# Optimization experiments

Hardware: AMD Instinct MI355X
Metric: run time of the kernel (lower is better)

## Reference

```python
import jax, jax.numpy as jnp
import numpy as np

CAPACITY = 65536
HIDDEN = 512
NUM_HASHES = 8
HASH_SIZE = 16
BATCH = 2048


def setup_inputs() -> dict:
    key = jax.random.key(0)
    ks = jax.random.split(key, 6)
    scale = 1.0 / np.sqrt(HIDDEN)
    query = jax.random.normal(ks[0], (BATCH, HIDDEN), dtype=jnp.float32)
    memory_keys = jax.random.normal(ks[1], (CAPACITY, HIDDEN), dtype=jnp.float32) * scale
    memory_values = jax.random.normal(ks[2], (CAPACITY, HIDDEN), dtype=jnp.float32) * scale
    hash_projections = jax.random.normal(ks[3], (NUM_HASHES, HIDDEN, HASH_SIZE), dtype=jnp.float32) * scale
    out_w = jax.random.normal(ks[4], (HIDDEN, HIDDEN), dtype=jnp.float32) * scale  # torch Linear weight [out,in]
    out_b = jnp.zeros((HIDDEN,), dtype=jnp.float32)
    return {"query": query, "memory_keys": memory_keys, "memory_values": memory_values,
            "hash_projections": hash_projections, "out_w": out_w, "out_b": out_b, "top_k": 32}


def _compute_hash(x, hash_projections):
    # x: [m, h] -> hash bits [m, num_hashes] in {0,1}
    # einsum 'bh,nhd->bnd' then sum over d then sign-threshold
    proj = jnp.einsum('mh,nhd->mnd', x, hash_projections)
    return (proj.sum(-1) > 0).astype(jnp.int32)


def reference(query, memory_keys, memory_values, hash_projections, out_w, out_b, top_k):
    b, h = query.shape
    q_hash = _compute_hash(query, hash_projections)                    # [b, n]
    k_hash = _compute_hash(memory_keys, hash_projections)              # [c, n] (no_grad in torch)
    # Hamming distance via +/-1 dot product: dot = n - 2*dist (avoids [b,c,n] bool tensor)
    qf = (q_hash * 2 - 1).astype(jnp.float32)
    kf = (k_hash * 2 - 1).astype(jnp.float32)
    dot = jnp.einsum('bn,cn->bc', qf, kf)                              # [b, c]
    hash_dist = ((NUM_HASHES - dot) * 0.5).astype(jnp.int32)           # [b, c]
    k = min(top_k, memory_keys.shape[0])
    _, top_indices = jax.lax.top_k(-hash_dist, k)                      # smallest distances, [b, k]
    selected_keys = memory_keys[top_indices]                           # [b, k, h]
    selected_values = memory_values[top_indices]                       # [b, k, h]
    scores = jnp.einsum('bh,bkh->bk', query, selected_keys) / np.sqrt(h).astype(np.float32)
    attn = jax.nn.softmax(scores, axis=-1)
    memory_output = jnp.einsum('bk,bkh->bh', attn, selected_values)    # [b, h]
    return memory_output @ out_w.T + out_b
```

## Files before the change

### kernel.cpp

```cpp
#include <hip/hip_runtime.h>
#include <stdint.h>

#define BATCH  2048
#define HID    512
#define CAP    65536
#define NHASH  8
#define TOPK   32
#define NSLICE 16
#define SLICE_SZ (CAP / NSLICE)
#define ROWS_TILE 16
#define QTILES (BATCH / ROWS_TILE)
#define KTILES (CAP / ROWS_TILE)
#define QGRID  128
#define KGRID  1024

typedef unsigned int   u32;
typedef unsigned long long u64;
typedef double d4 __attribute__((ext_vector_type(4)));

__global__ __launch_bounds__(256) void k_prep(const float* __restrict__ proj,
                                              double* __restrict__ psumT,
                                              u32* __restrict__ hist16,
                                              const float* __restrict__ w,
                                              float* __restrict__ wt) {
    __shared__ float tile[64][65];
    int bi = blockIdx.x, tid = threadIdx.x;
    if (bi < 2) {
        int g = bi * 256 + tid;
        for (int i = g; i < NSLICE * 256; i += 512) hist16[i] = 0;
        int h = g;
        for (int n = 0; n < NHASH; n++) {
            const float* p = proj + ((size_t)n * HID + h) * 16;
            double s = 0.0;
            #pragma unroll
            for (int d = 0; d < 16; d++) s += (double)p[d];
            psumT[(size_t)h * NHASH + n] = s;
        }
    } else {
        int b = bi - 2, bx = b & 7, by = b >> 3;
        int tx = tid & 63, ty = tid >> 6;
        for (int r = ty; r < 64; r += 4)
            tile[r][tx] = w[(size_t)(by * 64 + r) * HID + bx * 64 + tx];
        __syncthreads();
        for (int r = ty; r < 64; r += 4)
            wt[(size_t)(bx * 64 + r) * HID + by * 64 + tx] = tile[tx][r];
    }
}

__global__ __launch_bounds__(256, 3) void k_hash(const float* __restrict__ query,
                                                 const float* __restrict__ keys,
                                                 const double* __restrict__ psumT,
                                                 unsigned char* __restrict__ qhash,
                                                 unsigned char* __restrict__ khash,
                                                 u32* __restrict__ hist16) {
    __shared__ __align__(16) float sX[ROWS_TILE * HID];
    __shared__ double sAcc4[4][ROWS_TILE][8];

    const int tid  = threadIdx.x;
    const int w    = tid >> 6;
    const int m    = (tid & 63) & 15;
    const int kk   = (tid & 63) >> 4;

    const int isQ = (blockIdx.x < QGRID);
    const float* x        = isQ ? query : keys;
    unsigned char* outb   = isQ ? qhash : khash;
    const int nTiles      = isQ ? QTILES : KTILES;
    const int b0          = isQ ? blockIdx.x : (blockIdx.x - QGRID);
    const int gstride     = isQ ? QGRID : KGRID;
    const int do_hist     = !isQ;

    d4 z = {0.0, 0.0, 0.0, 0.0};
    d4 pr = __builtin_amdgcn_mfma_f64_16x16x4f64((double)(m + 1), 1.0, z, 0, 0, 0);
    d4 pc = __builtin_amdgcn_mfma_f64_16x16x4f64(1.0, (double)(m + 1), z, 0, 0, 0);
    d4 pp = __builtin_amdgcn_mfma_f64_16x16x4f64((double)(1 << kk),
                                                 (double)(1 << (4 * kk)), z, 0, 0, 0);
    int rowOf[4], colOf[4];
    #pragma unroll
    for (int i = 0; i < 4; i++) {
        rowOf[i] = (int)(pr[i] * 0.25) - 1;
        colOf[i] = (int)(pc[i] * 0.25) - 1;
    }
    u32 pb = (u32)pp[0];
    u32 pairPacked = 0;
    #pragma unroll
    for (int e = 0; e < 16; e++)
        if ((pb >> e) & 1u) pairPacked |= (u32)(e & 3) << (2 * (e >> 2));

    const int kAdj = (int)((pairPacked >> (2 * kk)) & 3u);
    double bfrag[32];
    #pragma unroll
    for (int j = 0; j < 32; j++) {
        int kp = 128 * w + 4 * j + kAdj;
        bfrag[j] = (m < 8) ? psumT[(size_t)kp * NHASH + m] : 0.0;
    }

    const int sw = (m & 7) << 2;

    for (int t = b0; t < nTiles; t += gstride) {
        const int rowBase = t * ROWS_TILE;

        for (int i = tid; i < ROWS_TILE * 128; i += 256) {
            int r = i >> 7, G = i & 127;
            float4 v = ((const float4*)(x + (size_t)(rowBase + r) * HID))[G];
            ((float4*)sX)[r * 128 + (G ^ (r & 7))] = v;
        }
        __syncthreads();

        d4 acc = {0.0, 0.0, 0.0, 0.0};
        const float* sxm = sX + m * HID;
        #pragma unroll
        for (int j = 0; j < 32; j++) {
            int k = 128 * w + 4 * j + kk;
            double a = (double)sxm[k ^ sw];
            acc = __builtin_amdgcn_mfma_f64_16x16x4f64(a, bfrag[j], acc, 0, 0, 0);
        }
        #pragma unroll
        for (int i = 0; i < 4; i++) {
            if (((unsigned)rowOf[i] < (unsigned)ROWS_TILE) && ((unsigned)colOf[i] < 8u))
                sAcc4[w][rowOf[i]][colOf[i]] = acc[i];
        }
        __syncthreads();

        if (tid < ROWS_TILE) {
            u32 byte = 0;
            #pragma unroll
            for (int n = 0; n < 8; n++) {
                double s = sAcc4[0][tid][n] + sAcc4[1][tid][n]
                         + sAcc4[2][tid][n] + sAcc4[3][tid][n];
                if (s > 0.0) byte |= (1u << n);
            }
            outb[rowBase + tid] = (unsigned char)byte;
            if (do_hist) atomicAdd(&hist16[((rowBase + tid) / SLICE_SZ) * 256 + byte], 1u);
        }
    }
}

__global__ __launch_bounds__(256) void k_scan(const u32* __restrict__ hist16,
                                              u32* __restrict__ bucketCnt,
                                              u32* __restrict__ bucketOff,
                                              u32* __restrict__ off16) {
    __shared__ u32 wsum[4];
    int v = threadIdx.x, lane = v & 63, wv = v >> 6;
    u32 tot = 0;
    for (int s = 0; s < NSLICE; s++) tot += hist16[s * 256 + v];
    bucketCnt[v] = tot;
    u32 inc = tot;
    #pragma unroll
    for (int s = 1; s < 64; s <<= 1) {
        u32 n = __shfl_up(inc, s, 64);
        if (lane >= s) inc += n;
    }
    if (lane == 63) wsum[wv] = inc;
    __syncthreads();
    u32 wof = 0;
    for (int i = 0; i < wv; i++) wof += wsum[i];
    u32 base = wof + inc - tot;
    bucketOff[v] = base;
    for (int s = 0; s < NSLICE; s++) { off16[s * 256 + v] = base; base += hist16[s * 256 + v]; }
}

__global__ __launch_bounds__(256) void k_compact(const unsigned char* __restrict__ khash,
                                                 const u32* __restrict__ off16,
                                                 u32* __restrict__ bucketList) {
    __shared__ unsigned char sh[SLICE_SZ];
    int s  = blockIdx.x & (NSLICE - 1);
    int bg = blockIdx.x >> 4;
    ((uint4*)sh)[threadIdx.x] = ((const uint4*)(khash + (size_t)s * SLICE_SZ))[threadIdx.x];
    __syncthreads();
    int w = threadIdx.x >> 6, lane = threadIdx.x & 63;
    int v = bg * 4 + w;
    u32 base = off16[s * 256 + v];
    for (int i = 0; i < SLICE_SZ / 64; i++) {
        int c = i * 64 + lane;
        unsigned char byte = sh[c];
        bool hit = (byte == (unsigned char)v);
        u64 m = __ballot(hit);
        if (hit) {
            int rank = __popcll(m & ((1ull << lane) - 1ull));
            bucketList[base + rank] = (u32)(s * SLICE_SZ + c);
        }
        base += (u32)__popcll(m);
    }
}

__global__ __launch_bounds__(256) void k_attn(const float* __restrict__ keys,
                                              const float* __restrict__ vals,
                                              const float* __restrict__ query,
                                              const unsigned char* __restrict__ qhash,
                                              const u32* __restrict__ bucketCnt,
                                              const u32* __restrict__ bucketOff,
                                              const u32* __restrict__ bucketList,
                                              float* __restrict__ mo) {
    __shared__ int sIdx[TOPK];
    __shared__ float sSc[TOPK], sE[TOPK];
    __shared__ int sPos0;
    int b = blockIdx.x, tid = threadIdx.x;
    int w = tid >> 6, lane = tid & 63;

    if (w == 0) {
        if (lane == 0) sPos0 = 0;
        u32 qh = qhash[b];

        int d[4]; u32 cnt[4], off[4];
        #pragma unroll
        for (int jj = 0; jj < 4; jj++) {
            int v = lane + jj * 64;
            d[jj] = __popc(qh ^ (u32)v);
            cnt[jj] = bucketCnt[v];
            off[jj] = bucketOff[v];
        }

        u32 ct[9];
        #pragma unroll
        for (int t = 0; t < 9; t++) {
            u32 c = 0;
            #pragma unroll
            for (int jj = 0; jj < 4; jj++) c += (d[jj] == t) ? cnt[jj] : 0u;
            #pragma unroll
            for (int s = 32; s >= 1; s >>= 1) c += __shfl_xor(c, s, 64);
            ct[t] = c;
        }

        int dcut = 0; u32 run = 0, before = 0;
        for (int t = 0; t < 9; t++) {
            before = run; run += ct[t];
            if (run >= TOPK) { dcut = t; break; }
        }
        int need = TOPK - (int)before;

        #pragma unroll
        for (int jj = 0; jj < 4; jj++) {
            if (d[jj] < dcut && cnt[jj] > 0) {
                int base = atomicAdd(&sPos0, (int)cnt[jj]);
                for (u32 e = 0; e < cnt[jj]; e++)
                    sIdx[base + e] = (int)bucketList[off[jj] + e];
            }
        }

        int nb = 0;
        #pragma unroll
        for (int jj = 0; jj < 4; jj++) nb += (d[jj] == dcut) ? 1 : 0;
        #pragma unroll
        for (int s = 32; s >= 1; s >>= 1) nb += __shfl_xor(nb, s, 64);

        if (nb == 1) {
            u32 boff = 0xFFFFFFFFu;
            #pragma unroll
            for (int jj = 0; jj < 4; jj++) if (d[jj] == dcut) boff = off[jj];
            #pragma unroll
            for (int s = 32; s >= 1; s >>= 1) boff = min(boff, __shfl_xor(boff, s, 64));
            if (lane < need)
                sIdx[(int)before + lane] = (int)bucketList[boff + lane];
        } else {
            u32 pos[4], end[4]; int val[4];
            #pragma unroll
            for (int jj = 0; jj < 4; jj++) {
                if (d[jj] == dcut && cnt[jj] > 0) {
                    pos[jj] = off[jj]; end[jj] = off[jj] + cnt[jj];
                    val[jj] = (int)bucketList[pos[jj]];
                } else { pos[jj] = 0; end[jj] = 0; val[jj] = 0x7fffffff; }
            }
            for (int it = 0; it < need; it++) {
                int m = min(min(val[0], val[1]), min(val[2], val[3]));
                int g = m;
                #pragma unroll
                for (int s = 32; s >= 1; s >>= 1) g = min(g, __shfl_xor(g, s, 64));
                if (lane == 0) sIdx[(int)before + it] = g;
                if (m == g && g != 0x7fffffff) {
                    #pragma unroll
                    for (int jj = 0; jj < 4; jj++) {
                        if (val[jj] == g) {
                            pos[jj]++;
                            val[jj] = (pos[jj] < end[jj]) ? (int)bucketList[pos[jj]] : 0x7fffffff;
                            break;
                        }
                    }
                }
            }
        }
    }
    __syncthreads();

    const float4* qp = (const float4*)(query + (size_t)b * HID + lane * 8);
    float4 qa = qp[0], qb = qp[1];

    for (int i = w * 8; i < w * 8 + 8; i++) {
        int idx = sIdx[i];
        const float4* kp = (const float4*)(keys + (size_t)idx * HID + lane * 8);
        float4 ka = kp[0], kb = kp[1];
        float dot = qa.x * ka.x + qa.y * ka.y + qa.z * ka.z + qa.w * ka.w
                  + qb.x * kb.x + qb.y * kb.y + qb.z * kb.z + qb.w * kb.w;
        #pragma unroll
        for (int s = 32; s >= 1; s >>= 1) dot += __shfl_xor(dot, s, 64);
        if (lane == 0) sSc[i] = dot * 0.04419417382415922f;
    }
    __syncthreads();

    if (tid < TOPK) {
        float m = -1e30f;
        for (int i = 0; i < TOPK; i++) m = fmaxf(m, sSc[i]);
        sE[tid] = expf(sSc[tid] - m);
    }
    __syncthreads();

    float sum = 0.f;
    for (int i = 0; i < TOPK; i++) sum += sE[i];
    float inv = 1.0f / sum;

    int h0 = tid * 2;
    float a0 = 0.f, a1 = 0.f;
    for (int i = 0; i < TOPK; i++) {
        int idx = sIdx[i];
        float e = sE[i];
        float2 vv = *(const float2*)(vals + (size_t)idx * HID + h0);
        a0 += e * vv.x; a1 += e * vv.y;
    }
    ((float2*)(mo + (size_t)b * HID))[tid] = make_float2(a0 * inv, a1 * inv);
}

__global__ __launch_bounds__(256) void k_proj(const float* __restrict__ mo,
                                              const float* __restrict__ wt,
                                              const float* __restrict__ bias,
                                              float* __restrict__ out) {
    int tid = threadIdx.x;
    int o = (blockIdx.x & 1) * 256 + tid;
    int bb = (blockIdx.x >> 1) * 8;
    float acc[8];
    #pragma unroll
    for (int r = 0; r < 8; r++) acc[r] = 0.f;
    for (int h = 0; h < HID; h++) {
        float wv = wt[(size_t)h * HID + o];
        #pragma unroll
        for (int r = 0; r < 8; r++)
            acc[r] += mo[(size_t)(bb + r) * HID + h] * wv;
    }
    float bv = bias[o];
    #pragma unroll
    for (int r = 0; r < 8; r++)
        out[(size_t)(bb + r) * HID + o] = acc[r] + bv;
}

extern "C" void kernel_launch(void* const* d_in, const int* in_sizes, int n_in,
                              void* d_out, int out_size, void* d_ws, size_t ws_size,
                              hipStream_t stream) {
    const float* query = (const float*)d_in[0];
    const float* keys  = (const float*)d_in[1];
    const float* vals  = (const float*)d_in[2];
    const float* proj  = (const float*)d_in[3];
    const float* outw  = (const float*)d_in[4];
    const float* outbp = (const float*)d_in[5];
    float* out = (float*)d_out;

    char* ws = (char*)d_ws;
    double*        psumT      = (double*)(ws + 0);
    unsigned char* qhash      = (unsigned char*)(ws + 32768);
    unsigned char* khash      = (unsigned char*)(ws + 34816);
    u32*           hist16     = (u32*)(ws + 100352);
    u32*           bucketCnt  = (u32*)(ws + 116736);
    u32*           bucketOff  = (u32*)(ws + 117760);
    u32*           off16      = (u32*)(ws + 118784);
    u32*           bucketList = (u32*)(ws + 135168);
    float*         mo         = (float*)(ws + 397312);
    float*         wt         = (float*)(ws + 4591616);
    (void)in_sizes; (void)n_in; (void)out_size; (void)ws_size;

    k_prep<<<66, 256, 0, stream>>>(proj, psumT, hist16, outw, wt);
    k_hash<<<QGRID + KGRID, 256, 0, stream>>>(query, keys, psumT, qhash, khash, hist16);
    k_scan<<<1, 256, 0, stream>>>(hist16, bucketCnt, bucketOff, off16);
    k_compact<<<1024, 256, 0, stream>>>(khash, off16, bucketList);
    k_attn<<<BATCH, 256, 0, stream>>>(keys, vals, query, qhash, bucketCnt, bucketOff, bucketList, mo);
    k_proj<<<512, 256, 0, stream>>>(mo, wt, outbp, out);
}
```

Before: 367.4 us.

## Prefetch next hash tile into registers and split MFMA accumulator chains

The hash kernel now handles query and key tiles through one unified tile index over a smaller persistent grid. Each block loads the next tile's rows into registers while it runs MFMAs on the current tile in shared memory, so global load latency overlaps compute. The single dependent MFMA accumulation chain is split into four independent accumulators that are summed at the end, which shortens the dependency stall. The cost is higher register pressure from the eight float4 prefetch registers plus the extra accumulators, which may lower occupancy.

```diff
diff --git a/kernel.cpp b/kernel.cpp
--- a/kernel.cpp
+++ b/kernel.cpp
@@ -11,8 +11,8 @@
 #define ROWS_TILE 16
 #define QTILES (BATCH / ROWS_TILE)
 #define KTILES (CAP / ROWS_TILE)
-#define QGRID  128
-#define KGRID  1024
+#define TOT_TILES (QTILES + KTILES)
+#define HGRID  768
 
 typedef unsigned int   u32;
 typedef unsigned long long u64;
@@ -61,14 +61,6 @@
     const int m    = (tid & 63) & 15;
     const int kk   = (tid & 63) >> 4;
 
-    const int isQ = (blockIdx.x < QGRID);
-    const float* x        = isQ ? query : keys;
-    unsigned char* outb   = isQ ? qhash : khash;
-    const int nTiles      = isQ ? QTILES : KTILES;
-    const int b0          = isQ ? blockIdx.x : (blockIdx.x - QGRID);
-    const int gstride     = isQ ? QGRID : KGRID;
-    const int do_hist     = !isQ;
-
     d4 z = {0.0, 0.0, 0.0, 0.0};
     d4 pr = __builtin_amdgcn_mfma_f64_16x16x4f64((double)(m + 1), 1.0, z, 0, 0, 0);
     d4 pc = __builtin_amdgcn_mfma_f64_16x16x4f64(1.0, (double)(m + 1), z, 0, 0, 0);
@@ -96,24 +88,54 @@
 
     const int sw = (m & 7) << 2;
 
-    for (int t = b0; t < nTiles; t += gstride) {
-        const int rowBase = t * ROWS_TILE;
-
-        for (int i = tid; i < ROWS_TILE * 128; i += 256) {
-            int r = i >> 7, G = i & 127;
-            float4 v = ((const float4*)(x + (size_t)(rowBase + r) * HID))[G];
-            ((float4*)sX)[r * 128 + (G ^ (r & 7))] = v;
+    float4 pf[8];
+
+    {
+        int tt = blockIdx.x;
+        const float* xb = (tt < QTILES)
+            ? (query + (size_t)tt * ROWS_TILE * HID)
+            : (keys + (size_t)(tt - QTILES) * ROWS_TILE * HID);
+        #pragma unroll
+        for (int p = 0; p < 8; p++) {
+            int i = tid + 256 * p, r = i >> 7, G = i & 127;
+            pf[p] = ((const float4*)(xb + (size_t)r * HID))[G];
+        }
+        #pragma unroll
+        for (int p = 0; p < 8; p++) {
+            int i = tid + 256 * p, r = i >> 7, G = i & 127;
+            ((float4*)sX)[r * 128 + (G ^ (r & 7))] = pf[p];
         }
         __syncthreads();
-
-        d4 acc = {0.0, 0.0, 0.0, 0.0};
+    }
+
+    int tt = blockIdx.x;
+    for (;;) {
+        const int tn = tt + HGRID;
+        const bool more = (tn < TOT_TILES);
+
+        if (more) {
+            const float* xb = (tn < QTILES)
+                ? (query + (size_t)tn * ROWS_TILE * HID)
+                : (keys + (size_t)(tn - QTILES) * ROWS_TILE * HID);
+            #pragma unroll
+            for (int p = 0; p < 8; p++) {
+                int i = tid + 256 * p, r = i >> 7, G = i & 127;
+                pf[p] = ((const float4*)(xb + (size_t)r * HID))[G];
+            }
+        }
+
+        d4 ac0 = z, ac1 = z, ac2 = z, ac3 = z;
         const float* sxm = sX + m * HID;
         #pragma unroll
-        for (int j = 0; j < 32; j++) {
-            int k = 128 * w + 4 * j + kk;
-            double a = (double)sxm[k ^ sw];
-            acc = __builtin_amdgcn_mfma_f64_16x16x4f64(a, bfrag[j], acc, 0, 0, 0);
-        }
+        for (int j8 = 0; j8 < 8; j8++) {
+            int k0 = 128 * w + ((4 * j8) ^ sw) + kk;
+            ac0 = __builtin_amdgcn_mfma_f64_16x16x4f64((double)sxm[k0],      bfrag[j8],      ac0, 0, 0, 0);
+            ac1 = __builtin_amdgcn_mfma_f64_16x16x4f64((double)sxm[k0 + 32], bfrag[j8 + 8],  ac1, 0, 0, 0);
+            ac2 = __builtin_amdgcn_mfma_f64_16x16x4f64((double)sxm[k0 + 64], bfrag[j8 + 16], ac2, 0, 0, 0);
+            ac3 = __builtin_amdgcn_mfma_f64_16x16x4f64((double)sxm[k0 + 96], bfrag[j8 + 24], ac3, 0, 0, 0);
+        }
+        d4 acc = (ac0 + ac1) + (ac2 + ac3);
+
         #pragma unroll
         for (int i = 0; i < 4; i++) {
             if (((unsigned)rowOf[i] < (unsigned)ROWS_TILE) && ((unsigned)colOf[i] < 8u))
@@ -129,9 +151,23 @@
                          + sAcc4[2][tid][n] + sAcc4[3][tid][n];
                 if (s > 0.0) byte |= (1u << n);
             }
-            outb[rowBase + tid] = (unsigned char)byte;
-            if (do_hist) atomicAdd(&hist16[((rowBase + tid) / SLICE_SZ) * 256 + byte], 1u);
-        }
+            if (tt < QTILES) {
+                qhash[tt * ROWS_TILE + tid] = (unsigned char)byte;
+            } else {
+                int row = (tt - QTILES) * ROWS_TILE + tid;
+                khash[row] = (unsigned char)byte;
+                atomicAdd(&hist16[(row / SLICE_SZ) * 256 + byte], 1u);
+            }
+        }
+        if (!more) break;
+
+        #pragma unroll
+        for (int p = 0; p < 8; p++) {
+            int i = tid + 256 * p, r = i >> 7, G = i & 127;
+            ((float4*)sX)[r * 128 + (G ^ (r & 7))] = pf[p];
+        }
+        __syncthreads();
+        tt = tn;
     }
 }
 
@@ -365,7 +401,7 @@
     (void)in_sizes; (void)n_in; (void)out_size; (void)ws_size;
 
     k_prep<<<66, 256, 0, stream>>>(proj, psumT, hist16, outw, wt);
-    k_hash<<<QGRID + KGRID, 256, 0, stream>>>(query, keys, psumT, qhash, khash, hist16);
+    k_hash<<<HGRID, 256, 0, stream>>>(query, keys, psumT, qhash, khash, hist16);
     k_scan<<<1, 256, 0, stream>>>(hist16, bucketCnt, bucketOff, off16);
     k_compact<<<1024, 256, 0, stream>>>(khash, off16, bucketList);
     k_attn<<<BATCH, 256, 0, stream>>>(keys, vals, query, qhash, bucketCnt, bucketOff, bucketList, mo);
```

After: 390.5 us. 6.3% more time.

## Rewrite hash kernel as one-wave-per-row FP64 FMA with shuffle reduction

Applied to the files above, without the earlier changes.

The hash kernel no longer stages 16-row tiles in LDS and runs f64 MFMA with block syncs. Instead each wavefront handles one row, keeping 64 precomputed projection sums per lane in registers. It does scalar FP64 FMAs, reduces across the wave with a butterfly shuffle and ballot, and prefetches the next row. This removes the LDS traffic and barriers and shrinks the grid to 512 blocks, at the cost of higher register pressure and moving FP64 work from the matrix units to vector FMAs.

```diff
diff --git a/kernel.cpp b/kernel.cpp
--- a/kernel.cpp
+++ b/kernel.cpp
@@ -8,15 +8,11 @@
 #define TOPK   32
 #define NSLICE 16
 #define SLICE_SZ (CAP / NSLICE)
-#define ROWS_TILE 16
-#define QTILES (BATCH / ROWS_TILE)
-#define KTILES (CAP / ROWS_TILE)
-#define QGRID  128
-#define KGRID  1024
+#define NROWS  (BATCH + CAP)
+#define HGRID  512
 
 typedef unsigned int   u32;
 typedef unsigned long long u64;
-typedef double d4 __attribute__((ext_vector_type(4)));
 
 __global__ __launch_bounds__(256) void k_prep(const float* __restrict__ proj,
                                               double* __restrict__ psumT,
@@ -47,91 +43,115 @@
     }
 }
 
-__global__ __launch_bounds__(256, 3) void k_hash(const float* __restrict__ query,
+__global__ __launch_bounds__(256, 2) void k_hash(const float* __restrict__ query,
                                                  const float* __restrict__ keys,
                                                  const double* __restrict__ psumT,
                                                  unsigned char* __restrict__ qhash,
                                                  unsigned char* __restrict__ khash,
                                                  u32* __restrict__ hist16) {
-    __shared__ __align__(16) float sX[ROWS_TILE * HID];
-    __shared__ double sAcc4[4][ROWS_TILE][8];
-
-    const int tid  = threadIdx.x;
-    const int w    = tid >> 6;
-    const int m    = (tid & 63) & 15;
-    const int kk   = (tid & 63) >> 4;
-
-    const int isQ = (blockIdx.x < QGRID);
-    const float* x        = isQ ? query : keys;
-    unsigned char* outb   = isQ ? qhash : khash;
-    const int nTiles      = isQ ? QTILES : KTILES;
-    const int b0          = isQ ? blockIdx.x : (blockIdx.x - QGRID);
-    const int gstride     = isQ ? QGRID : KGRID;
-    const int do_hist     = !isQ;
-
-    d4 z = {0.0, 0.0, 0.0, 0.0};
-    d4 pr = __builtin_amdgcn_mfma_f64_16x16x4f64((double)(m + 1), 1.0, z, 0, 0, 0);
-    d4 pc = __builtin_amdgcn_mfma_f64_16x16x4f64(1.0, (double)(m + 1), z, 0, 0, 0);
-    d4 pp = __builtin_amdgcn_mfma_f64_16x16x4f64((double)(1 << kk),
-                                                 (double)(1 << (4 * kk)), z, 0, 0, 0);
-    int rowOf[4], colOf[4];
-    #pragma unroll
-    for (int i = 0; i < 4; i++) {
-        rowOf[i] = (int)(pr[i] * 0.25) - 1;
-        colOf[i] = (int)(pc[i] * 0.25) - 1;
-    }
-    u32 pb = (u32)pp[0];
-    u32 pairPacked = 0;
-    #pragma unroll
-    for (int e = 0; e < 16; e++)
-        if ((pb >> e) & 1u) pairPacked |= (u32)(e & 3) << (2 * (e >> 2));
-
-    const int kAdj = (int)((pairPacked >> (2 * kk)) & 3u);
-    double bfrag[32];
-    #pragma unroll
-    for (int j = 0; j < 32; j++) {
-        int kp = 128 * w + 4 * j + kAdj;
-        bfrag[j] = (m < 8) ? psumT[(size_t)kp * NHASH + m] : 0.0;
-    }
-
-    const int sw = (m & 7) << 2;
-
-    for (int t = b0; t < nTiles; t += gstride) {
-        const int rowBase = t * ROWS_TILE;
-
-        for (int i = tid; i < ROWS_TILE * 128; i += 256) {
-            int r = i >> 7, G = i & 127;
-            float4 v = ((const float4*)(x + (size_t)(rowBase + r) * HID))[G];
-            ((float4*)sX)[r * 128 + (G ^ (r & 7))] = v;
-        }
-        __syncthreads();
-
-        d4 acc = {0.0, 0.0, 0.0, 0.0};
-        const float* sxm = sX + m * HID;
-        #pragma unroll
-        for (int j = 0; j < 32; j++) {
-            int k = 128 * w + 4 * j + kk;
-            double a = (double)sxm[k ^ sw];
-            acc = __builtin_amdgcn_mfma_f64_16x16x4f64(a, bfrag[j], acc, 0, 0, 0);
-        }
+    const int lane = threadIdx.x & 63;
+    const int W    = (blockIdx.x << 2) | (threadIdx.x >> 6);
+    const int NW   = HGRID << 2;
+
+    double P[8][8];
+    {
+        const double* pp = psumT + ((size_t)lane << 6);
+        #pragma unroll
+        for (int j = 0; j < 8; j++)
+            #pragma unroll
+            for (int n = 0; n < 8; n++)
+                P[j][n] = pp[j * 8 + n];
+    }
+
+    const int sel1 = lane & 1, sel2 = (lane >> 1) & 1, sel3 = (lane >> 2) & 1;
+
+    int r = W;
+    float4 xa, xb;
+    if (r < NROWS) {
+        const float* xp = (r < BATCH) ? (query + (size_t)r * HID)
+                                      : (keys + (size_t)(r - BATCH) * HID);
+        const float4* v4 = (const float4*)xp + (lane << 1);
+        xa = v4[0]; xb = v4[1];
+    }
+    while (r < NROWS) {
+        const int rn = r + NW;
+        float4 na, nb;
+        if (rn < NROWS) {
+            const float* xp = (rn < BATCH) ? (query + (size_t)rn * HID)
+                                           : (keys + (size_t)(rn - BATCH) * HID);
+            const float4* v4 = (const float4*)xp + (lane << 1);
+            na = v4[0]; nb = v4[1];
+        }
+
+        double acc[8];
+        #pragma unroll
+        for (int n = 0; n < 8; n++) acc[n] = 0.0;
+        {
+            float xf0 = xa.x, xf1 = xa.y, xf2 = xa.z, xf3 = xa.w;
+            float xf4 = xb.x, xf5 = xb.y, xf6 = xb.z, xf7 = xb.w;
+            double xd;
+            xd = (double)xf0;
+            #pragma unroll
+            for (int n = 0; n < 8; n++) acc[n] = fma(xd, P[0][n], acc[n]);
+            xd = (double)xf1;
+            #pragma unroll
+            for (int n = 0; n < 8; n++) acc[n] = fma(xd, P[1][n], acc[n]);
+            xd = (double)xf2;
+            #pragma unroll
+            for (int n = 0; n < 8; n++) acc[n] = fma(xd, P[2][n], acc[n]);
+            xd = (double)xf3;
+            #pragma unroll
+            for (int n = 0; n < 8; n++) acc[n] = fma(xd, P[3][n], acc[n]);
+            xd = (double)xf4;
+            #pragma unroll
+            for (int n = 0; n < 8; n++) acc[n] = fma(xd, P[4][n], acc[n]);
+            xd = (double)xf5;
+            #pragma unroll
+            for (int n = 0; n < 8; n++) acc[n] = fma(xd, P[5][n], acc[n]);
+            xd = (double)xf6;
+            #pragma unroll
+            for (int n = 0; n < 8; n++) acc[n] = fma(xd, P[6][n], acc[n]);
+            xd = (double)xf7;
+            #pragma unroll
+            for (int n = 0; n < 8; n++) acc[n] = fma(xd, P[7][n], acc[n]);
+        }
+
+        double t4[4];
         #pragma unroll
         for (int i = 0; i < 4; i++) {
-            if (((unsigned)rowOf[i] < (unsigned)ROWS_TILE) && ((unsigned)colOf[i] < 8u))
-                sAcc4[w][rowOf[i]][colOf[i]] = acc[i];
-        }
-        __syncthreads();
-
-        if (tid < ROWS_TILE) {
-            u32 byte = 0;
-            #pragma unroll
-            for (int n = 0; n < 8; n++) {
-                double s = sAcc4[0][tid][n] + sAcc4[1][tid][n]
-                         + sAcc4[2][tid][n] + sAcc4[3][tid][n];
-                if (s > 0.0) byte |= (1u << n);
+            double a0 = acc[2 * i], a1 = acc[2 * i + 1];
+            double keep = sel1 ? a1 : a0;
+            double give = sel1 ? a0 : a1;
+            t4[i] = keep + __shfl_xor(give, 1, 64);
+        }
+        double t2[2];
+        #pragma unroll
+        for (int i = 0; i < 2; i++) {
+            double a0 = t4[2 * i], a1 = t4[2 * i + 1];
+            double keep = sel2 ? a1 : a0;
+            double give = sel2 ? a0 : a1;
+            t2[i] = keep + __shfl_xor(give, 2, 64);
+        }
+        double keep = sel3 ? t2[1] : t2[0];
+        double give = sel3 ? t2[0] : t2[1];
+        double v = keep + __shfl_xor(give, 4, 64);
+        v += __shfl_xor(v, 8, 64);
+        v += __shfl_xor(v, 16, 64);
+        v += __shfl_xor(v, 32, 64);
+
+        u64 bm = __ballot(v > 0.0);
+        if (lane == 0) {
+            u32 byte = (u32)(bm & 0xFFull);
+            if (r < BATCH) {
+                qhash[r] = (unsigned char)byte;
+            } else {
+                int kr = r - BATCH;
+                khash[kr] = (unsigned char)byte;
+                atomicAdd(&hist16[(kr >> 12) * 256 + byte], 1u);
             }
-            outb[rowBase + tid] = (unsigned char)byte;
-            if (do_hist) atomicAdd(&hist16[((rowBase + tid) / SLICE_SZ) * 256 + byte], 1u);
-        }
+        }
+        xa = na; xb = nb;
+        r = rn;
     }
 }
 
@@ -365,7 +385,7 @@
     (void)in_sizes; (void)n_in; (void)out_size; (void)ws_size;
 
     k_prep<<<66, 256, 0, stream>>>(proj, psumT, hist16, outw, wt);
-    k_hash<<<QGRID + KGRID, 256, 0, stream>>>(query, keys, psumT, qhash, khash, hist16);
+    k_hash<<<HGRID, 256, 0, stream>>>(query, keys, psumT, qhash, khash, hist16);
     k_scan<<<1, 256, 0, stream>>>(hist16, bucketCnt, bucketOff, off16);
     k_compact<<<1024, 256, 0, stream>>>(khash, off16, bucketList);
     k_attn<<<BATCH, 256, 0, stream>>>(keys, vals, query, qhash, bucketCnt, bucketOff, bucketList, mo);
```

New measurement: 362.5 us. Within noise of the previous version (-1.3%).
